# Performance work log

Hardware: AMD Instinct MI355X
Metric: run time of the kernel (lower is better)

Reference implementation:

```python
import jax, jax.numpy as jnp
import numpy as np

E, M, IN, OUT = 8, 8192, 2048, 8192


def setup_inputs() -> dict:
    key = jax.random.key(0)
    k1, k2, k3 = jax.random.split(key, 3)
    inputs = jax.random.normal(k1, (M, IN), dtype=jnp.float32)
    # truncated_normal(-3,3) scaled by init_scale/sqrt(In), matching MoELinear.init
    weight = jax.random.truncated_normal(k2, -3.0, 3.0, (E, IN, OUT), dtype=jnp.float32) * (1.0 / np.sqrt(IN))
    bias = jax.random.normal(k3, (OUT,), dtype=jnp.float32) * 0.02
    # tokens are pre-sorted by expert; balanced routing: M/E tokens per expert
    group_sizes = jnp.full((E,), M // E, dtype=jnp.int32)
    return {"inputs": inputs, "weight": weight, "group_sizes": group_sizes, "bias": bias}


def _ragged_matmul(inputs, weight, group_sizes):
    """Grouped GEMM: out[m] = inputs[m] @ weight[expert_of(m)].

    Tokens are contiguous per expert; group_sizes[e] gives the count for
    expert e. Same math as jax.lax.ragged_dot / megablox gmm.
    """
    n_experts = weight.shape[0]
    m = inputs.shape[0]
    # static-length repeat -> per-token expert id, jit-safe
    expert_ids = jnp.repeat(jnp.arange(n_experts, dtype=group_sizes.dtype),
                            group_sizes, total_repeat_length=m)  # [M]

    def body(acc, ew):
        e, w = ew  # w: [In, Out]
        mask = (expert_ids == e).astype(inputs.dtype)  # [M]
        return acc + (inputs * mask[:, None]) @ w, None

    acc0 = jnp.zeros((m, weight.shape[2]), dtype=inputs.dtype)
    out, _ = jax.lax.scan(body, acc0, (jnp.arange(n_experts, dtype=group_sizes.dtype), weight))
    return out


def reference(inputs, weight, group_sizes, bias):
    # MoELinear.__call__ (ragged_dot path): grouped matmul + bias
    return _ragged_matmul(inputs, weight, group_sizes) + bias
```

## Files before the change

kernel.cpp:

```cpp
#include <hip/hip_runtime.h>
#include <stdint.h>

#define E_ 8
#define M_ 8192
#define K_ 2048
#define N_ 8192

#define BM 256
#define BN 256
#define BK 64
#define NT (K_ / BK)
#define LDS_BYTES 131072

typedef __attribute__((ext_vector_type(8))) short bf16x8;
typedef __attribute__((ext_vector_type(4))) float f32x4;
typedef __attribute__((ext_vector_type(8))) unsigned short us8;

__device__ __forceinline__ unsigned short f2bf(float f) {
  union { float f; uint32_t u; } v; v.f = f;
  uint32_t u = v.u;
  uint32_t r = (u + 0x7FFFu + ((u >> 16) & 1u)) >> 16;
  return (unsigned short)r;
}

__device__ __forceinline__ void gload_lds16(const void* g, void* l) {
  __builtin_amdgcn_global_load_lds(
      (const __attribute__((address_space(1))) unsigned int*)g,
      (__attribute__((address_space(3))) unsigned int*)l,
      16, 0, 0);
}

__global__ __launch_bounds__(256) void conv_a(const float* __restrict__ A,
                                              unsigned short* __restrict__ Ab,
                                              int n8) {
  int stride = gridDim.x * blockDim.x;
  for (int idx = blockIdx.x * blockDim.x + threadIdx.x; idx < n8; idx += stride) {
    const float4* p = reinterpret_cast<const float4*>(A) + (size_t)idx * 2;
    float4 x0 = p[0], x1 = p[1];
    us8 o;
    o[0] = f2bf(x0.x); o[1] = f2bf(x0.y); o[2] = f2bf(x0.z); o[3] = f2bf(x0.w);
    o[4] = f2bf(x1.x); o[5] = f2bf(x1.y); o[6] = f2bf(x1.z); o[7] = f2bf(x1.w);
    *reinterpret_cast<us8*>(Ab + (size_t)idx * 8) = o;
  }
}

__global__ __launch_bounds__(256) void conv_wT(const float* __restrict__ W,
                                               unsigned short* __restrict__ Wt,
                                               int e_fixed) {
  __shared__ float t[64][65];
  int tid = threadIdx.x;
  int tx = tid & 63, ty = tid >> 6;
  int n0 = blockIdx.x * 64, k0 = blockIdx.y * 64;
  int e = (gridDim.z > 1) ? blockIdx.z : e_fixed;
  size_t win = (size_t)e * K_ * N_;
  size_t wout = (gridDim.z > 1) ? win : 0;

  #pragma unroll
  for (int r = 0; r < 16; ++r) {
    int kl = r * 4 + ty;
    t[kl][tx] = W[win + (size_t)(k0 + kl) * N_ + n0 + tx];
  }
  __syncthreads();
  int px = tid & 31, py = tid >> 5;
  #pragma unroll
  for (int r = 0; r < 8; ++r) {
    int nl = r * 8 + py;
    unsigned int pack = (unsigned int)f2bf(t[2 * px][nl]) |
                        ((unsigned int)f2bf(t[2 * px + 1][nl]) << 16);
    *reinterpret_cast<unsigned int*>(Wt + wout + (size_t)(n0 + nl) * K_ + k0 + 2 * px) = pack;
  }
}

__global__ __launch_bounds__(512, 2) void moe_gemm_bf16(
    const unsigned short* __restrict__ Ab,
    const unsigned short* __restrict__ Wt,
    const int* __restrict__ gs,
    const float* __restrict__ bias,
    float* __restrict__ C,
    int only_expert, size_t wt_stride) {
  extern __shared__ char smem[];

  int tile_n = blockIdx.x;
  int tile_m = blockIdx.y;

  int expert = -1, row_start = 0, rows = 0;
  if (only_expert >= 0) {
    int off = 0;
    for (int e = 0; e < only_expert; ++e) off += gs[e];
    int g = gs[only_expert];
    int t0 = tile_m * BM;
    if (t0 >= g) return;
    expert = only_expert;
    row_start = off + t0;
    rows = min(BM, g - t0);
  } else {
    int acc = 0, off = 0;
    for (int e = 0; e < E_; ++e) {
      int g = gs[e];
      int t = (g + BM - 1) / BM;
      if (expert < 0 && tile_m < acc + t) {
        int lt = tile_m - acc;
        expert = e;
        row_start = off + lt * BM;
        rows = min(BM, g - lt * BM);
      }
      acc += t;
      off += g;
    }
    if (expert < 0) return;
  }

  const unsigned short* WtE = Wt + (size_t)expert * wt_stride;

  int tid = threadIdx.x;
  int lane = tid & 63;
  int wave = tid >> 6;
  int wr = wave >> 2;
  int wc = wave & 3;
  int bh = wc >> 1;
  int ln15 = lane & 15;
  int n0 = tile_n * BN;

  int sl16 = (((lane >> 4) ^ ((ln15 & 3) ^ ((ln15 >> 2) & 3))) << 4);
  int aRB = wr * 16384 + ln15 * 64 + sl16;
  int bRB = 32768 + bh * 16384 + ((wc & 1) * 64 + ln15) * 64 + sl16;

  int soff = tid * 16;
  int srow = soff >> 6;
  int sslot = (soff >> 4) & 3;
  int skc = sslot ^ ((srow & 3) ^ ((srow >> 2) & 3));
  int scol0 = skc * 8;

  const unsigned short* aS[2][2];
  const unsigned short* bS[2][2];
  #pragma unroll
  for (int h = 0; h < 2; ++h) {
    int r = h * 128 + srow;
    int gr = r < rows ? r : 0;
    #pragma unroll
    for (int ks = 0; ks < 2; ++ks) {
      aS[h][ks] = Ab + (size_t)(row_start + gr) * K_ + ks * 32 + scol0;
      bS[h][ks] = WtE + (size_t)(n0 + h * 128 + srow) * K_ + ks * 32 + scol0;
    }
  }

#define STG_A(DB, h, ks, kt) \
  gload_lds16(aS[h][ks] + (kt) * 64, smem + (DB) + (h) * 16384 + (ks) * 8192 + soff)
#define STG_B(DB, h, ks, kt) \
  gload_lds16(bS[h][ks] + (kt) * 64, smem + (DB) + 32768 + (h) * 16384 + (ks) * 8192 + soff)

  f32x4 acc4[8][4];
  #pragma unroll
  for (int i = 0; i < 8; ++i)
    #pragma unroll
    for (int j = 0; j < 4; ++j)
      acc4[i][j] = f32x4{0.f, 0.f, 0.f, 0.f};

  STG_A(0, 0, 0, 0); STG_A(0, 1, 0, 0);
  STG_B(0, 0, 0, 0); STG_B(0, 1, 0, 0);
  STG_A(0, 0, 1, 0); STG_A(0, 1, 1, 0);
  STG_B(0, 0, 1, 0); STG_B(0, 1, 1, 0);

#define ITER(T, DB, DBN)                                                      \
  do {                                                                        \
    int ktn = (T) + 1; if (ktn >= NT) ktn = 0;                                \
    asm volatile("s_waitcnt vmcnt(4)" ::: "memory");                          \
    __builtin_amdgcn_s_barrier();                                             \
    bf16x8 a0[4], b0[4], a1[4];                                               \
    _Pragma("unroll") for (int mi = 0; mi < 4; ++mi)                          \
      a0[mi] = *(const bf16x8*)(smem + (DB) + aRB + mi * 1024);               \
    _Pragma("unroll") for (int nj = 0; nj < 4; ++nj)                          \
      b0[nj] = *(const bf16x8*)(smem + (DB) + bRB + nj * 1024);               \
    STG_A(DBN, 0, 0, ktn); STG_A(DBN, 1, 0, ktn);                             \
    asm volatile("s_waitcnt lgkmcnt(0)" ::: "memory");                        \
    __builtin_amdgcn_sched_barrier(0);                                        \
    __builtin_amdgcn_s_setprio(1);                                            \
    _Pragma("unroll") for (int mi = 0; mi < 4; ++mi)                          \
      _Pragma("unroll") for (int nj = 0; nj < 4; ++nj)                        \
        acc4[mi][nj] = __builtin_amdgcn_mfma_f32_16x16x32_bf16(               \
            a0[mi], b0[nj], acc4[mi][nj], 0, 0, 0);                           \
    __builtin_amdgcn_s_setprio(0);                                            \
    _Pragma("unroll") for (int mi = 0; mi < 4; ++mi)                          \
      a1[mi] = *(const bf16x8*)(smem + (DB) + aRB + (mi + 4) * 1024);         \
    STG_B(DBN, 0, 0, ktn); STG_B(DBN, 1, 0, ktn);                             \
    asm volatile("s_waitcnt lgkmcnt(0)" ::: "memory");                        \
    __builtin_amdgcn_sched_barrier(0);                                        \
    __builtin_amdgcn_s_setprio(1);                                            \
    _Pragma("unroll") for (int mi = 0; mi < 4; ++mi)                          \
      _Pragma("unroll") for (int nj = 0; nj < 4; ++nj)                        \
        acc4[mi + 4][nj] = __builtin_amdgcn_mfma_f32_16x16x32_bf16(           \
            a1[mi], b0[nj], acc4[mi + 4][nj], 0, 0, 0);                       \
    __builtin_amdgcn_s_setprio(0);                                            \
    asm volatile("s_waitcnt vmcnt(4)" ::: "memory");                          \
    __builtin_amdgcn_s_barrier();                                             \
    _Pragma("unroll") for (int mi = 0; mi < 4; ++mi)                          \
      a0[mi] = *(const bf16x8*)(smem + (DB) + aRB + 8192 + mi * 1024);        \
    _Pragma("unroll") for (int nj = 0; nj < 4; ++nj)                          \
      b0[nj] = *(const bf16x8*)(smem + (DB) + bRB + 8192 + nj * 1024);        \
    STG_A(DBN, 0, 1, ktn); STG_A(DBN, 1, 1, ktn);                             \
    asm volatile("s_waitcnt lgkmcnt(0)" ::: "memory");                        \
    __builtin_amdgcn_sched_barrier(0);                                        \
    __builtin_amdgcn_s_setprio(1);                                            \
    _Pragma("unroll") for (int mi = 0; mi < 4; ++mi)                          \
      _Pragma("unroll") for (int nj = 0; nj < 4; ++nj)                        \
        acc4[mi][nj] = __builtin_amdgcn_mfma_f32_16x16x32_bf16(               \
            a0[mi], b0[nj], acc4[mi][nj], 0, 0, 0);                           \
    __builtin_amdgcn_s_setprio(0);                                            \
    _Pragma("unroll") for (int mi = 0; mi < 4; ++mi)                          \
      a1[mi] = *(const bf16x8*)(smem + (DB) + aRB + 8192 + (mi + 4) * 1024);  \
    STG_B(DBN, 0, 1, ktn); STG_B(DBN, 1, 1, ktn);                             \
    asm volatile("s_waitcnt lgkmcnt(0)" ::: "memory");                        \
    __builtin_amdgcn_sched_barrier(0);                                        \
    __builtin_amdgcn_s_setprio(1);                                            \
    _Pragma("unroll") for (int mi = 0; mi < 4; ++mi)                          \
      _Pragma("unroll") for (int nj = 0; nj < 4; ++nj)                        \
        acc4[mi + 4][nj] = __builtin_amdgcn_mfma_f32_16x16x32_bf16(           \
            a1[mi], b0[nj], acc4[mi + 4][nj], 0, 0, 0);                       \
    __builtin_amdgcn_s_setprio(0);                                            \
  } while (0)

  for (int t2 = 0; t2 < NT; t2 += 2) {
    ITER(t2, 0, 65536);
    ITER(t2 + 1, 65536, 0);
  }
#undef ITER
#undef STG_A
#undef STG_B

  asm volatile("s_waitcnt vmcnt(0)" ::: "memory");

  float bv[4];
  #pragma unroll
  for (int nj = 0; nj < 4; ++nj) bv[nj] = bias[n0 + wc * 64 + nj * 16 + ln15];
  #pragma unroll
  for (int mi = 0; mi < 8; ++mi) {
    int r0 = wr * 128 + mi * 16 + (lane >> 4) * 4;
    #pragma unroll
    for (int r = 0; r < 4; ++r) {
      int lr = r0 + r;
      if (lr < rows) {
        float* Cp = C + (size_t)(row_start + lr) * N_ + n0 + wc * 64 + ln15;
        #pragma unroll
        for (int nj = 0; nj < 4; ++nj) Cp[nj * 16] = acc4[mi][nj][r] + bv[nj];
      }
    }
  }
}

__global__ __launch_bounds__(256) void moe_naive(const float* __restrict__ A,
                                                 const float* __restrict__ W,
                                                 const int* __restrict__ gs,
                                                 const float* __restrict__ bias,
                                                 float* __restrict__ C) {
  int col = blockIdx.x * 16 + (threadIdx.x & 15);
  int row = blockIdx.y * 16 + (threadIdx.x >> 4);
  int acc = 0, e = E_ - 1;
  for (int i = 0; i < E_; ++i) {
    int g = gs[i];
    if (row >= acc && row < acc + g) { e = i; break; }
    acc += g;
  }
  const float* a = A + (size_t)row * K_;
  const float* w = W + (size_t)e * K_ * N_ + col;
  float s = 0.f;
  for (int k = 0; k < K_; ++k) s += a[k] * w[(size_t)k * N_];
  C[(size_t)row * N_ + col] = s + bias[col];
}

extern "C" void kernel_launch(void* const* d_in, const int* in_sizes, int n_in,
                              void* d_out, int out_size, void* d_ws, size_t ws_size,
                              hipStream_t stream) {
  const float* A = (const float*)d_in[0];
  const float* W = (const float*)d_in[1];
  const int* gs = (const int*)d_in[2];
  const float* bias = (const float*)d_in[3];
  float* C = (float*)d_out;

  const size_t needA = (size_t)M_ * K_ * 2;
  const size_t needWall = (size_t)E_ * K_ * N_ * 2;
  const size_t needW1 = (size_t)K_ * N_ * 2;

  (void)hipFuncSetAttribute((const void*)moe_gemm_bf16,
                            hipFuncAttributeMaxDynamicSharedMemorySize, LDS_BYTES);

  if (ws_size >= needA + needWall) {
    unsigned short* Abf = (unsigned short*)d_ws;
    unsigned short* Wtb = (unsigned short*)((char*)d_ws + needA);
    conv_a<<<2048, 256, 0, stream>>>(A, Abf, (M_ * K_) / 8);
    dim3 gw(N_ / 64, K_ / 64, E_);
    conv_wT<<<gw, 256, 0, stream>>>(W, Wtb, 0);
    dim3 gg(N_ / BN, M_ / BM + E_);
    moe_gemm_bf16<<<gg, 512, LDS_BYTES, stream>>>(Abf, Wtb, gs, bias, C, -1, (size_t)N_ * K_);
  } else if (ws_size >= needA + needW1) {
    unsigned short* Abf = (unsigned short*)d_ws;
    unsigned short* Wtb = (unsigned short*)((char*)d_ws + needA);
    conv_a<<<2048, 256, 0, stream>>>(A, Abf, (M_ * K_) / 8);
    for (int e = 0; e < E_; ++e) {
      dim3 gw(N_ / 64, K_ / 64, 1);
      conv_wT<<<gw, 256, 0, stream>>>(W, Wtb, e);
      dim3 gg(N_ / BN, M_ / BM);
      moe_gemm_bf16<<<gg, 512, LDS_BYTES, stream>>>(Abf, Wtb, gs, bias, C, e, 0);
    }
  } else {
    dim3 gn(N_ / 16, M_ / 16);
    moe_naive<<<gn, 256, 0, stream>>>(A, W, gs, bias, C);
  }
}
```

Before: 444.2 us.

## Restructure main loop into four-phase ping-pong schedule with interleaved A/B staging

Reorganizes the K-loop so each half-tile issues one A and one B global-to-LDS stage per phase, with extra workgroup barriers between LDS fragment reads and MFMA blocks. The wait on outstanding vector memory moves to the end of each k-half, and the prologue waits before the loop starts. The goal is to interleave global loads, LDS reads and MFMA across waves in a ping-pong style to hide latency. In exchange it adds more s_barrier calls per iteration, which could add synchronization overhead, and the changed vmcnt placement has to stay correct for the double-buffer hazards.

New measurement: 460.0 us. 3.6% more time.

```diff
diff --git a/kernel.cpp b/kernel.cpp
--- a/kernel.cpp
+++ b/kernel.cpp
@@ -156,74 +156,76 @@
     for (int j = 0; j < 4; ++j)
       acc4[i][j] = f32x4{0.f, 0.f, 0.f, 0.f};
 
-  STG_A(0, 0, 0, 0); STG_A(0, 1, 0, 0);
-  STG_B(0, 0, 0, 0); STG_B(0, 1, 0, 0);
-  STG_A(0, 0, 1, 0); STG_A(0, 1, 1, 0);
-  STG_B(0, 0, 1, 0); STG_B(0, 1, 1, 0);
-
-#define ITER(T, DB, DBN)                                                      \
+#define DS_A(frag, DB, KS, MIBASE)                                            \
+  _Pragma("unroll") for (int mi = 0; mi < 4; ++mi)                            \
+    frag[mi] = *(const bf16x8*)(smem + (DB) + aRB + (KS) * 8192 +             \
+                                ((MIBASE) + mi) * 1024);
+#define DS_B(frag, DB, KS)                                                    \
+  _Pragma("unroll") for (int nj = 0; nj < 4; ++nj)                            \
+    frag[nj] = *(const bf16x8*)(smem + (DB) + bRB + (KS) * 8192 + nj * 1024);
+#define MFMA16(MB, af, bf)                                                    \
+  __builtin_amdgcn_s_setprio(1);                                              \
+  _Pragma("unroll") for (int mi = 0; mi < 4; ++mi)                            \
+    _Pragma("unroll") for (int nj = 0; nj < 4; ++nj)                          \
+      acc4[(MB) + mi][nj] = __builtin_amdgcn_mfma_f32_16x16x32_bf16(          \
+          af[mi], bf[nj], acc4[(MB) + mi][nj], 0, 0, 0);                      \
+  __builtin_amdgcn_s_setprio(0);
+
+#define TILE4(DB, DBN, KTN)                                                   \
   do {                                                                        \
-    int ktn = (T) + 1; if (ktn >= NT) ktn = 0;                                \
-    asm volatile("s_waitcnt vmcnt(4)" ::: "memory");                          \
-    __builtin_amdgcn_s_barrier();                                             \
-    bf16x8 a0[4], b0[4], a1[4];                                               \
-    _Pragma("unroll") for (int mi = 0; mi < 4; ++mi)                          \
-      a0[mi] = *(const bf16x8*)(smem + (DB) + aRB + mi * 1024);               \
-    _Pragma("unroll") for (int nj = 0; nj < 4; ++nj)                          \
-      b0[nj] = *(const bf16x8*)(smem + (DB) + bRB + nj * 1024);               \
-    STG_A(DBN, 0, 0, ktn); STG_A(DBN, 1, 0, ktn);                             \
+    bf16x8 af[4], bf[4];                                                      \
+                                              \
+    DS_A(af, DB, 0, 0); DS_B(bf, DB, 0);                                      \
+    STG_A(DBN, 0, 0, KTN); STG_B(DBN, 0, 0, KTN);                             \
+    __builtin_amdgcn_s_barrier();                                             \
     asm volatile("s_waitcnt lgkmcnt(0)" ::: "memory");                        \
     __builtin_amdgcn_sched_barrier(0);                                        \
-    __builtin_amdgcn_s_setprio(1);                                            \
-    _Pragma("unroll") for (int mi = 0; mi < 4; ++mi)                          \
-      _Pragma("unroll") for (int nj = 0; nj < 4; ++nj)                        \
-        acc4[mi][nj] = __builtin_amdgcn_mfma_f32_16x16x32_bf16(               \
-            a0[mi], b0[nj], acc4[mi][nj], 0, 0, 0);                           \
-    __builtin_amdgcn_s_setprio(0);                                            \
-    _Pragma("unroll") for (int mi = 0; mi < 4; ++mi)                          \
-      a1[mi] = *(const bf16x8*)(smem + (DB) + aRB + (mi + 4) * 1024);         \
-    STG_B(DBN, 0, 0, ktn); STG_B(DBN, 1, 0, ktn);                             \
+    MFMA16(0, af, bf);                                                        \
+    __builtin_amdgcn_s_barrier();                                             \
+                                    \
+    DS_A(af, DB, 0, 4);                                                       \
+    STG_A(DBN, 1, 0, KTN); STG_B(DBN, 1, 0, KTN);                             \
+    __builtin_amdgcn_s_barrier();                                             \
     asm volatile("s_waitcnt lgkmcnt(0)" ::: "memory");                        \
     __builtin_amdgcn_sched_barrier(0);                                        \
-    __builtin_amdgcn_s_setprio(1);                                            \
-    _Pragma("unroll") for (int mi = 0; mi < 4; ++mi)                          \
-      _Pragma("unroll") for (int nj = 0; nj < 4; ++nj)                        \
-        acc4[mi + 4][nj] = __builtin_amdgcn_mfma_f32_16x16x32_bf16(           \
-            a1[mi], b0[nj], acc4[mi + 4][nj], 0, 0, 0);                       \
-    __builtin_amdgcn_s_setprio(0);                                            \
+    MFMA16(4, af, bf);                                                        \
     asm volatile("s_waitcnt vmcnt(4)" ::: "memory");                          \
     __builtin_amdgcn_s_barrier();                                             \
-    _Pragma("unroll") for (int mi = 0; mi < 4; ++mi)                          \
-      a0[mi] = *(const bf16x8*)(smem + (DB) + aRB + 8192 + mi * 1024);        \
-    _Pragma("unroll") for (int nj = 0; nj < 4; ++nj)                          \
-      b0[nj] = *(const bf16x8*)(smem + (DB) + bRB + 8192 + nj * 1024);        \
-    STG_A(DBN, 0, 1, ktn); STG_A(DBN, 1, 1, ktn);                             \
+                                              \
+    DS_A(af, DB, 1, 0); DS_B(bf, DB, 1);                                      \
+    STG_A(DBN, 0, 1, KTN); STG_B(DBN, 0, 1, KTN);                             \
+    __builtin_amdgcn_s_barrier();                                             \
     asm volatile("s_waitcnt lgkmcnt(0)" ::: "memory");                        \
     __builtin_amdgcn_sched_barrier(0);                                        \
-    __builtin_amdgcn_s_setprio(1);                                            \
-    _Pragma("unroll") for (int mi = 0; mi < 4; ++mi)                          \
-      _Pragma("unroll") for (int nj = 0; nj < 4; ++nj)                        \
-        acc4[mi][nj] = __builtin_amdgcn_mfma_f32_16x16x32_bf16(               \
-            a0[mi], b0[nj], acc4[mi][nj], 0, 0, 0);                           \
-    __builtin_amdgcn_s_setprio(0);                                            \
-    _Pragma("unroll") for (int mi = 0; mi < 4; ++mi)                          \
-      a1[mi] = *(const bf16x8*)(smem + (DB) + aRB + 8192 + (mi + 4) * 1024);  \
-    STG_B(DBN, 0, 1, ktn); STG_B(DBN, 1, 1, ktn);                             \
+    MFMA16(0, af, bf);                                                        \
+    __builtin_amdgcn_s_barrier();                                             \
+                                                       \
+    DS_A(af, DB, 1, 4);                                                       \
+    STG_A(DBN, 1, 1, KTN); STG_B(DBN, 1, 1, KTN);                             \
+    __builtin_amdgcn_s_barrier();                                             \
     asm volatile("s_waitcnt lgkmcnt(0)" ::: "memory");                        \
     __builtin_amdgcn_sched_barrier(0);                                        \
-    __builtin_amdgcn_s_setprio(1);                                            \
-    _Pragma("unroll") for (int mi = 0; mi < 4; ++mi)                          \
-      _Pragma("unroll") for (int nj = 0; nj < 4; ++nj)                        \
-        acc4[mi + 4][nj] = __builtin_amdgcn_mfma_f32_16x16x32_bf16(           \
-            a1[mi], b0[nj], acc4[mi + 4][nj], 0, 0, 0);                       \
-    __builtin_amdgcn_s_setprio(0);                                            \
+    MFMA16(4, af, bf);                                                        \
+    asm volatile("s_waitcnt vmcnt(4)" ::: "memory");                          \
+    __builtin_amdgcn_s_barrier();                                             \
   } while (0)
 
+  STG_A(0, 0, 0, 0); STG_B(0, 0, 0, 0);
+  STG_A(0, 1, 0, 0); STG_B(0, 1, 0, 0);
+  STG_A(0, 0, 1, 0); STG_B(0, 0, 1, 0);
+  STG_A(0, 1, 1, 0); STG_B(0, 1, 1, 0);
+  asm volatile("s_waitcnt vmcnt(4)" ::: "memory");
+  __builtin_amdgcn_s_barrier();
+
   for (int t2 = 0; t2 < NT; t2 += 2) {
-    ITER(t2, 0, 65536);
-    ITER(t2 + 1, 65536, 0);
-  }
-#undef ITER
+    int ktn2 = (t2 + 2 >= NT) ? 0 : t2 + 2;
+    TILE4(0, 65536, t2 + 1);
+    TILE4(65536, 0, ktn2);
+  }
+#undef TILE4
+#undef DS_A
+#undef DS_B
+#undef MFMA16
 #undef STG_A
 #undef STG_B
 
```
